# Optimization experiments

Measured on AMD Instinct MI355X. Metric: run time of the kernel, lower is better.

The kernel has to match this reference:

```python
import math
import jax, jax.numpy as jnp
import numpy as np

EPS = 1e-5
NUM_HEADER = 2


def pos_encoding(C, T, dtype):
    i = jnp.arange(C)
    exp = -((i - (i % 2)).astype(dtype) / C)
    freqs = jnp.power(jnp.asarray(10000.0, dtype), exp)[:, None]      # [C,1]
    phases = ((i % 2).astype(dtype) * (np.pi / 2))[:, None]           # [C,1]
    pos = jnp.arange(T, dtype=dtype)[None, :]                         # [1,T]
    return jnp.sin(pos * freqs + phases)                              # [C,T]


def layernorm2d(x, g, b):
    # LayerNorm over (C,T) jointly, per batch element (nn.LayerNorm([C, length]))
    mu = jnp.mean(x, axis=(1, 2), keepdims=True)
    var = jnp.mean((x - mu) ** 2, axis=(1, 2), keepdims=True)
    return (x - mu) * jax.lax.rsqrt(var + EPS) * g[None] + b[None]


def dsconv(x, dw_w, dw_b, pw_w, pw_b):
    # depthwise conv1d (groups=C, 'same' padding for odd k) + pointwise 1x1
    C = x.shape[1]
    k = dw_w.shape[-1]
    y = jax.lax.conv_general_dilated(
        x, dw_w[:, None, :], (1,), [(k // 2, k // 2)],
        dimension_numbers=('NCH', 'OIH', 'NCH'), feature_group_count=C)
    y = y + dw_b[None, :, None]
    y = jnp.einsum('bct,oc->bot', y, pw_w) + pw_b[None, :, None]
    return y


def attention(x, mask, Wq, Wk, Wv, Wo):
    # Faithful to source bug: all heads use Wqs[1]/Wks[1]/Wvs[1] -> identical heads.
    xt = jnp.transpose(x, (0, 2, 1))          # [B,T,C]
    C = xt.shape[-1]
    dk = C / NUM_HEADER
    q = xt @ Wq                               # [B,T,dk]
    k_ = xt @ Wk
    v = xt @ Wv
    s = jnp.einsum('bqd,bkd->bqk', q, k_) * (1.0 / math.sqrt(dk))
    hmask = mask[:, None, :]                  # mask over keys
    s = s * hmask + (1 - hmask) * (-1e30)
    a = jax.nn.softmax(s, axis=2) * mask[:, :, None]
    head = a @ v                              # [B,T,dk]
    heads = jnp.tile(head, (1, 1, NUM_HEADER))  # concat of identical heads
    out = heads @ Wo                          # [B,T,C]
    return jnp.transpose(out, (0, 2, 1))      # [B,C,T]


def setup_inputs() -> dict:
    key = jax.random.key(0)
    B, C, T = 16, 128, 1024
    NCONV, K = 4, 7
    dk = C // NUM_HEADER
    ks = jax.random.split(key, 12)
    inp = {
        'x': jax.random.normal(ks[0], (B, C, T), jnp.float32),
        'mask': jnp.ones((B, T), jnp.float32),
        'dw_w': jax.random.normal(ks[1], (NCONV, C, K), jnp.float32) * math.sqrt(2.0 / K),
        'dw_b': jnp.zeros((NCONV, C), jnp.float32),
        'pw_w': jax.random.normal(ks[2], (NCONV, C, C), jnp.float32) * math.sqrt(2.0 / C),
        'pw_b': jnp.zeros((NCONV, C), jnp.float32),
        'norm0_g': jnp.ones((C, T), jnp.float32),
        'norm0_b': jnp.zeros((C, T), jnp.float32),
        'norms_g': jnp.ones((NCONV, C, T), jnp.float32),
        'norms_b': jnp.zeros((NCONV, C, T), jnp.float32),
        'norme_g': jnp.ones((C, T), jnp.float32),
        'norme_b': jnp.zeros((C, T), jnp.float32),
        'Wq': jax.random.normal(ks[3], (C, dk), jnp.float32) * math.sqrt(2.0 / (C + dk)),
        'Wk': jax.random.normal(ks[4], (C, dk), jnp.float32) * math.sqrt(2.0 / (C + dk)),
        'Wv': jax.random.normal(ks[5], (C, dk), jnp.float32) * math.sqrt(2.0 / (C + dk)),
        'Wo': jax.random.normal(ks[6], (C, C), jnp.float32) * math.sqrt(2.0 / C),
        'fc_w': jax.random.normal(ks[7], (C, C), jnp.float32) * (0.1 * math.sqrt(6.0 / (2 * C))),
        'fc_b': jnp.zeros((C,), jnp.float32),
    }
    return inp


def reference(x, mask, dw_w, dw_b, pw_w, pw_b, norm0_g, norm0_b,
              norms_g, norms_b, norme_g, norme_b,
              Wq, Wk, Wv, Wo, fc_w, fc_b):
    B, C, T = x.shape
    nconv = dw_w.shape[0]
    # dropout is identity in eval mode (reference is deterministic)
    out = x + pos_encoding(C, T, x.dtype)[None]
    res = layernorm2d(out, norm0_g, norm0_b)
    for i in range(nconv):
        out = dsconv(out, dw_w[i], dw_b[i], pw_w[i], pw_b[i])
        out = jax.nn.relu(out)
        out = out + res
        res = out
        out = layernorm2d(out, norms_g[i], norms_b[i])
    out = attention(out, mask, Wq, Wk, Wv, Wo)
    out = out + res
    res = out
    out = layernorm2d(out, norme_g, norme_b)
    out = jnp.einsum('bct,oc->bot', out, fc_w) + fc_b[None, :, None]
    out = jax.nn.relu(out)
    out = out + res
    return out
```

## Files before the change

kernel.cpp:

```cpp
#include <hip/hip_runtime.h>
#include <math.h>

#define BB 16
#define CC 128
#define TT 1024
#define KK 7
#define DK 64
#define NSPLIT 4

typedef float f32x4 __attribute__((ext_vector_type(4)));
typedef short s16x8 __attribute__((ext_vector_type(8)));

__device__ inline short f2bf(float f) {
  union { float f; unsigned u; } v; v.f = f;
  unsigned r = (v.u + 0x7FFFu + ((v.u >> 16) & 1u)) >> 16;
  return (short)r;
}

__device__ inline float bf2f(short s) {
  union { unsigned u; float f; } v;
  v.u = ((unsigned)(unsigned short)s) << 16;
  return v.f;
}

__device__ inline void block_partial_256(float s, float ss, float* dst) {
#pragma unroll
  for (int off = 32; off; off >>= 1) { s += __shfl_xor(s, off); ss += __shfl_xor(ss, off); }
  __shared__ float red[8];
  int w = threadIdx.x >> 6;
  if ((threadIdx.x & 63) == 0) { red[2 * w] = s; red[2 * w + 1] = ss; }
  __syncthreads();
  if (threadIdx.x == 0) {
    for (int i = 1; i < 4; ++i) { s += red[2 * i]; ss += red[2 * i + 1]; }
    dst[0] = s; dst[1] = ss;
  }
}

__device__ inline void ln_stats_from_parts(const float* part_batch, int n, float* sh) {
  if (threadIdx.x < 64) {
    float s = 0.f, ss = 0.f;
    for (int i = threadIdx.x; i < n; i += 64) { s += part_batch[2 * i]; ss += part_batch[2 * i + 1]; }
#pragma unroll
    for (int off = 32; off; off >>= 1) { s += __shfl_xor(s, off); ss += __shfl_xor(ss, off); }
    if (threadIdx.x == 0) {
      const float invN = 1.f / (float)(CC * TT);
      float mu = s * invN;
      sh[0] = mu;
      sh[1] = rsqrtf(ss * invN - mu * mu + 1e-5f);
    }
  }
  __syncthreads();
}

__global__ __launch_bounds__(256) void k_prep(const float* __restrict__ pww,
                                              const float* __restrict__ Wq,
                                              const float* __restrict__ Wk,
                                              const float* __restrict__ Wv,
                                              const float* __restrict__ Wo,
                                              const float* __restrict__ fcw,
                                              short* __restrict__ pwwb,
                                              short* __restrict__ wqkvb,
                                              short* __restrict__ wo2b,
                                              short* __restrict__ fcwb) {
  int i = blockIdx.x * 256 + threadIdx.x;
  if (i < 65536) { pwwb[i] = f2bf(pww[i]); return; }
  i -= 65536;
  if (i < 24576) {
    int m = i >> 7, c = i & 127;
    int sel = m >> 6, d = m & 63;
    const float* srcp = sel == 0 ? Wq : (sel == 1 ? Wk : Wv);
    wqkvb[i] = f2bf(srcp[c * DK + d]);
    return;
  }
  i -= 24576;
  if (i < 8192) {
    int o = i >> 6, d = i & 63;
    wo2b[i] = f2bf(Wo[d * CC + o] + Wo[(d + 64) * CC + o]);
    return;
  }
  i -= 8192;
  fcwb[i] = f2bf(fcw[i]);
}

__global__ __launch_bounds__(256) void k_addpos(const float* __restrict__ x,
                                                float* __restrict__ out,
                                                float* __restrict__ part) {
  int bc = blockIdx.x;
  int c = bc & (CC - 1);
  float ce = (float)(c & ~1);
  float freq = expf(-(ce / (float)CC) * 9.210340371976184f);
  float phase = (c & 1) ? 1.5707963267948966f : 0.0f;
  const float* xr = x + (size_t)bc * TT;
  float* orow = out + (size_t)bc * TT;
  int t = threadIdx.x * 4;
  float4 v = *(const float4*)(xr + t);
  v.x += sinf((float)(t + 0) * freq + phase);
  v.y += sinf((float)(t + 1) * freq + phase);
  v.z += sinf((float)(t + 2) * freq + phase);
  v.w += sinf((float)(t + 3) * freq + phase);
  *(float4*)(orow + t) = v;
  float s = v.x + v.y + v.z + v.w;
  float ss = v.x * v.x + v.y * v.y + v.z * v.z + v.w * v.w;
  block_partial_256(s, ss, part + (size_t)bc * 2);
}

template <bool LN_IN, bool LN_RES>
__global__ __launch_bounds__(256) void k_dsconv(const float* __restrict__ in,
                                                const float* __restrict__ lng,
                                                const float* __restrict__ lnb,
                                                const float* __restrict__ part_in, int npart,
                                                const float* __restrict__ dww,
                                                const float* __restrict__ dwb,
                                                const short* __restrict__ pwwb,
                                                const float* __restrict__ pwb,
                                                float* __restrict__ out,
                                                float* __restrict__ part_out) {
  int tile = blockIdx.x & 31, b = blockIdx.x >> 5;
  int t0 = tile * 32;
  __shared__ float stats[2];
  __shared__ float xs[CC][41];
  __shared__ float xr2[LN_IN ? CC : 1][33];
  __shared__ __align__(16) short Dt[32][136];
  ln_stats_from_parts(part_in + (size_t)b * npart * 2, npart, stats);
  float mu = stats[0], rs = stats[1];

  for (int i = threadIdx.x; i < CC * 10; i += 256) {
    int c = i / 10, q = i - c * 10;
    int tb = t0 - 4 + q * 4;
    const float* rowp = in + ((size_t)b * CC + c) * TT;
    float r0, r1, r2, r3, o0, o1, o2, o3;
    bool full = (tb >= 0) && (tb + 4 <= TT);
    if (full) {
      float4 v = *(const float4*)(rowp + tb);
      r0 = v.x; r1 = v.y; r2 = v.z; r3 = v.w;
      o0 = r0; o1 = r1; o2 = r2; o3 = r3;
      if (LN_IN) {
        float4 g = *(const float4*)(lng + (size_t)c * TT + tb);
        float4 bv = *(const float4*)(lnb + (size_t)c * TT + tb);
        o0 = (r0 - mu) * rs * g.x + bv.x;
        o1 = (r1 - mu) * rs * g.y + bv.y;
        o2 = (r2 - mu) * rs * g.z + bv.z;
        o3 = (r3 - mu) * rs * g.w + bv.w;
      }
    } else {
      float rr[4], oo[4];
#pragma unroll
      for (int k = 0; k < 4; ++k) {
        int t = tb + k;
        bool inb = (t >= 0) && (t < TT);
        float rv = inb ? rowp[t] : 0.f;
        rr[k] = rv;
        float ov = rv;
        if (LN_IN && inb)
          ov = (rv - mu) * rs * lng[(size_t)c * TT + t] + lnb[(size_t)c * TT + t];
        oo[k] = ov;
      }
      r0 = rr[0]; r1 = rr[1]; r2 = rr[2]; r3 = rr[3];
      o0 = oo[0]; o1 = oo[1]; o2 = oo[2]; o3 = oo[3];
    }
    if (LN_IN && q >= 1 && q <= 8) {
      int tl = (q - 1) * 4;
      xr2[c][tl] = r0; xr2[c][tl + 1] = r1; xr2[c][tl + 2] = r2; xr2[c][tl + 3] = r3;
    }
    int base = q * 4;
    xs[c][base] = o0; xs[c][base + 1] = o1; xs[c][base + 2] = o2; xs[c][base + 3] = o3;
  }
  __syncthreads();
  for (int i = threadIdx.x; i < 32 * CC; i += 256) {
    int t = i >> 7, c = i & 127;
    float a = dwb[c];
#pragma unroll
    for (int j = 0; j < KK; ++j) a += dww[c * KK + j] * xs[c][t + j + 1];
    Dt[t][c] = f2bf(a);
  }
  __syncthreads();

  int w = threadIdx.x >> 6, lane = threadIdx.x & 63;
  int lo = lane & 15, hi = lane >> 4;
  f32x4 acc[2][2];
#pragma unroll
  for (int mt = 0; mt < 2; ++mt)
#pragma unroll
    for (int nt = 0; nt < 2; ++nt) { acc[mt][nt][0] = 0.f; acc[mt][nt][1] = 0.f; acc[mt][nt][2] = 0.f; acc[mt][nt][3] = 0.f; }
#pragma unroll
  for (int ks = 0; ks < 4; ++ks) {
    s16x8 b0 = *(const s16x8*)&Dt[lo][ks * 32 + hi * 8];
    s16x8 b1 = *(const s16x8*)&Dt[16 + lo][ks * 32 + hi * 8];
    s16x8 a0 = *(const s16x8*)&pwwb[(size_t)(w * 32 + lo) * CC + ks * 32 + hi * 8];
    s16x8 a1 = *(const s16x8*)&pwwb[(size_t)(w * 32 + 16 + lo) * CC + ks * 32 + hi * 8];
    acc[0][0] = __builtin_amdgcn_mfma_f32_16x16x32_bf16(a0, b0, acc[0][0], 0, 0, 0);
    acc[0][1] = __builtin_amdgcn_mfma_f32_16x16x32_bf16(a0, b1, acc[0][1], 0, 0, 0);
    acc[1][0] = __builtin_amdgcn_mfma_f32_16x16x32_bf16(a1, b0, acc[1][0], 0, 0, 0);
    acc[1][1] = __builtin_amdgcn_mfma_f32_16x16x32_bf16(a1, b1, acc[1][1], 0, 0, 0);
  }

  float s = 0.f, ss = 0.f;
#pragma unroll
  for (int mt = 0; mt < 2; ++mt)
#pragma unroll
    for (int nt = 0; nt < 2; ++nt)
#pragma unroll
      for (int r = 0; r < 4; ++r) {
        int row = w * 32 + mt * 16 + hi * 4 + r;
        int tl = nt * 16 + lo;
        int t = t0 + tl;
        float v = acc[mt][nt][r] + pwb[row];
        v = v > 0.f ? v : 0.f;
        float rv;
        if (LN_RES) {
          float raw = xs[row][tl + 4];
          rv = (raw - mu) * rs * lng[row * TT + t] + lnb[row * TT + t];
        } else if (LN_IN) {
          rv = xr2[row][tl];
        } else {
          rv = xs[row][tl + 4];
        }
        v += rv;
        out[((size_t)b * CC + row) * TT + t] = v;
        s += v; ss += v * v;
      }
  block_partial_256(s, ss, part_out + (size_t)blockIdx.x * 2);
}

__global__ __launch_bounds__(256) void k_qkv(const float* __restrict__ in,
                                             const float* __restrict__ lng,
                                             const float* __restrict__ lnb,
                                             const float* __restrict__ part_in,
                                             const short* __restrict__ wqkvb,
                                             short* __restrict__ q,
                                             short* __restrict__ k,
                                             short* __restrict__ vt) {
  int tile = blockIdx.x & 31, b = blockIdx.x >> 5;
  int t0 = tile * 32;
  __shared__ float stats[2];
  __shared__ __align__(16) short Dt[32][136];
  ln_stats_from_parts(part_in + (size_t)b * 64, 32, stats);
  float mu = stats[0], rs = stats[1];
  for (int i = threadIdx.x; i < CC * 8; i += 256) {
    int c = i >> 3, qq = i & 7;
    int t = qq * 4;
    size_t off = (size_t)c * TT + t0 + t;
    float4 v = *(const float4*)(in + (size_t)b * CC * TT + off);
    float4 g = *(const float4*)(lng + off);
    float4 bb = *(const float4*)(lnb + off);
    Dt[t + 0][c] = f2bf((v.x - mu) * rs * g.x + bb.x);
    Dt[t + 1][c] = f2bf((v.y - mu) * rs * g.y + bb.y);
    Dt[t + 2][c] = f2bf((v.z - mu) * rs * g.z + bb.z);
    Dt[t + 3][c] = f2bf((v.w - mu) * rs * g.w + bb.w);
  }
  __syncthreads();

  int w = threadIdx.x >> 6, lane = threadIdx.x & 63;
  int lo = lane & 15, hi = lane >> 4;
  f32x4 acc[3][2];
#pragma unroll
  for (int mt = 0; mt < 3; ++mt)
#pragma unroll
    for (int nt = 0; nt < 2; ++nt) { acc[mt][nt][0] = 0.f; acc[mt][nt][1] = 0.f; acc[mt][nt][2] = 0.f; acc[mt][nt][3] = 0.f; }
#pragma unroll
  for (int ks = 0; ks < 4; ++ks) {
    s16x8 b0 = *(const s16x8*)&Dt[lo][ks * 32 + hi * 8];
    s16x8 b1 = *(const s16x8*)&Dt[16 + lo][ks * 32 + hi * 8];
#pragma unroll
    for (int mt = 0; mt < 3; ++mt) {
      s16x8 a = *(const s16x8*)&wqkvb[(size_t)(w * 48 + mt * 16 + lo) * CC + ks * 32 + hi * 8];
      acc[mt][0] = __builtin_amdgcn_mfma_f32_16x16x32_bf16(a, b0, acc[mt][0], 0, 0, 0);
      acc[mt][1] = __builtin_amdgcn_mfma_f32_16x16x32_bf16(a, b1, acc[mt][1], 0, 0, 0);
    }
  }
#pragma unroll
  for (int mt = 0; mt < 3; ++mt)
#pragma unroll
    for (int nt = 0; nt < 2; ++nt) {
      int m0 = w * 48 + mt * 16 + hi * 4;
      int t = t0 + nt * 16 + lo;
      short4 pk;
      pk.x = f2bf(acc[mt][nt][0]); pk.y = f2bf(acc[mt][nt][1]);
      pk.z = f2bf(acc[mt][nt][2]); pk.w = f2bf(acc[mt][nt][3]);
      if (m0 < 64) {
        *(short4*)(q + ((size_t)b * TT + t) * DK + m0) = pk;
      } else if (m0 < 128) {
        *(short4*)(k + ((size_t)b * TT + t) * DK + (m0 - 64)) = pk;
      } else {
        int d = m0 - 128;
        vt[((size_t)b * DK + d) * TT + t] = pk.x;
        vt[((size_t)b * DK + d + 1) * TT + t] = pk.y;
        vt[((size_t)b * DK + d + 2) * TT + t] = pk.z;
        vt[((size_t)b * DK + d + 3) * TT + t] = pk.w;
      }
    }
}

__global__ __launch_bounds__(128) void k_attn(const short* __restrict__ qb,
                                              const short* __restrict__ kbuf,
                                              const short* __restrict__ vtb,
                                              const float* __restrict__ mask,
                                              short* __restrict__ pacch,
                                              float* __restrict__ pml) {
  int sp = blockIdx.x & (NSPLIT - 1);
  int qt = (blockIdx.x >> 2) & 31;
  int b = blockIdx.x >> 7;
  int w = threadIdx.x >> 6, lane = threadIdx.x & 63;
  int lo = lane & 15, hi = lane >> 4;

  __shared__ __align__(16) short ks[64][72];
  __shared__ __align__(16) short vt[64][72];
  __shared__ __align__(16) short ps[2][16][68];
  __shared__ float ms[64];

  const short* qp = qb + ((size_t)b * TT + qt * 32 + w * 16 + lo) * DK + hi * 8;
  s16x8 aq0 = *(const s16x8*)qp;
  s16x8 aq1 = *(const s16x8*)(qp + 32);

  f32x4 acc[4];
  float m_i[4], l_i[4];
#pragma unroll
  for (int r = 0; r < 4; ++r) {
    m_i[r] = -3.0e38f; l_i[r] = 0.f;
#pragma unroll
    for (int nt = 0; nt < 4; ++nt) acc[nt][r] = 0.f;
  }
  const float scale = 0.125f;

  for (int kb2 = sp * (TT / 64 / NSPLIT); kb2 < (sp + 1) * (TT / 64 / NSPLIT); ++kb2) {
    __syncthreads();
    for (int i = threadIdx.x; i < 512; i += 128) {
      int r = i >> 3, ch = i & 7;
      *(s16x8*)&ks[r][ch * 8] =
          *(const s16x8*)(kbuf + ((size_t)b * TT + kb2 * 64 + r) * DK + ch * 8);
      *(s16x8*)&vt[r][ch * 8] =
          *(const s16x8*)(vtb + ((size_t)b * DK + r) * TT + kb2 * 64 + ch * 8);
    }
    if (threadIdx.x < 64) ms[threadIdx.x] = mask[(size_t)b * TT + kb2 * 64 + threadIdx.x];
    __syncthreads();

    f32x4 sc[4];
#pragma unroll
    for (int nt = 0; nt < 4; ++nt) {
      f32x4 z; z[0] = 0.f; z[1] = 0.f; z[2] = 0.f; z[3] = 0.f;
      s16x8 bk0 = *(const s16x8*)&ks[nt * 16 + lo][hi * 8];
      s16x8 bk1 = *(const s16x8*)&ks[nt * 16 + lo][32 + hi * 8];
      z = __builtin_amdgcn_mfma_f32_16x16x32_bf16(aq0, bk0, z, 0, 0, 0);
      z = __builtin_amdgcn_mfma_f32_16x16x32_bf16(aq1, bk1, z, 0, 0, 0);
      sc[nt] = z;
    }
#pragma unroll
    for (int nt = 0; nt < 4; ++nt) {
      float mv = ms[nt * 16 + lo];
      float addv = (1.f - mv) * -1e30f;
#pragma unroll
      for (int r = 0; r < 4; ++r) sc[nt][r] = sc[nt][r] * scale * mv + addv;
    }
    float alpha[4];
#pragma unroll
    for (int r = 0; r < 4; ++r) {
      float m0 = fmaxf(fmaxf(sc[0][r], sc[1][r]), fmaxf(sc[2][r], sc[3][r]));
#pragma unroll
      for (int off = 1; off < 16; off <<= 1) m0 = fmaxf(m0, __shfl_xor(m0, off));
      float mn = fmaxf(m_i[r], m0);
      alpha[r] = __expf(m_i[r] - mn);
      m_i[r] = mn;
    }
    float psum[4] = {0.f, 0.f, 0.f, 0.f};
#pragma unroll
    for (int nt = 0; nt < 4; ++nt)
#pragma unroll
      for (int r = 0; r < 4; ++r) {
        float p = __expf(sc[nt][r] - m_i[r]);
        psum[r] += p;
        ps[w][hi * 4 + r][nt * 16 + lo] = f2bf(p);
      }
#pragma unroll
    for (int r = 0; r < 4; ++r) {
      float sum = psum[r];
#pragma unroll
      for (int off = 1; off < 16; off <<= 1) sum += __shfl_xor(sum, off);
      l_i[r] = l_i[r] * alpha[r] + sum;
    }
#pragma unroll
    for (int nt = 0; nt < 4; ++nt)
#pragma unroll
      for (int r = 0; r < 4; ++r) acc[nt][r] *= alpha[r];

    s16x8 ap0 = *(const s16x8*)&ps[w][lo][hi * 8];
    s16x8 ap1 = *(const s16x8*)&ps[w][lo][32 + hi * 8];
#pragma unroll
    for (int nt = 0; nt < 4; ++nt) {
      s16x8 bv0 = *(const s16x8*)&vt[nt * 16 + lo][hi * 8];
      s16x8 bv1 = *(const s16x8*)&vt[nt * 16 + lo][32 + hi * 8];
      acc[nt] = __builtin_amdgcn_mfma_f32_16x16x32_bf16(ap0, bv0, acc[nt], 0, 0, 0);
      acc[nt] = __builtin_amdgcn_mfma_f32_16x16x32_bf16(ap1, bv1, acc[nt], 0, 0, 0);
    }
  }
#pragma unroll
  for (int r = 0; r < 4; ++r) {
    int row = qt * 32 + w * 16 + hi * 4 + r;
    size_t pb = (((size_t)b * TT + row) * NSPLIT + sp) * DK;
#pragma unroll
    for (int nt = 0; nt < 4; ++nt) pacch[pb + nt * 16 + lo] = f2bf(acc[nt][r]);
    if (lo == 0) {
      size_t mb = (((size_t)b * TT + row) * NSPLIT + sp) * 2;
      pml[mb] = m_i[r];
      pml[mb + 1] = l_i[r];
    }
  }
}

__global__ __launch_bounds__(256) void k_attnout2(const short* __restrict__ pacch,
                                                  const float* __restrict__ pml,
                                                  const float* __restrict__ mask,
                                                  const short* __restrict__ wo2b,
                                                  const float* __restrict__ res,
                                                  float* __restrict__ out,
                                                  float* __restrict__ part_out) {
  int tile = blockIdx.x & 31, b = blockIdx.x >> 5;
  int t0 = tile * 32;
  __shared__ __align__(16) short Ht[32][72];
  {
    int i = threadIdx.x;
    int tr = i >> 3, q = i & 7;
    size_t rb = (size_t)b * TT + t0 + tr;
    float m[NSPLIT], l[NSPLIT];
#pragma unroll
    for (int s = 0; s < NSPLIT; ++s) {
      m[s] = pml[(rb * NSPLIT + s) * 2];
      l[s] = pml[(rb * NSPLIT + s) * 2 + 1];
    }
    float M = fmaxf(fmaxf(m[0], m[1]), fmaxf(m[2], m[3]));
    float wgt[NSPLIT], L = 0.f;
#pragma unroll
    for (int s = 0; s < NSPLIT; ++s) { wgt[s] = __expf(m[s] - M); L += wgt[s] * l[s]; }
    float inv = mask[rb] / L;
    float o[8] = {0.f, 0.f, 0.f, 0.f, 0.f, 0.f, 0.f, 0.f};
#pragma unroll
    for (int s = 0; s < NSPLIT; ++s) {
      s16x8 pv = *(const s16x8*)(pacch + (rb * NSPLIT + s) * DK + q * 8);
#pragma unroll
      for (int j = 0; j < 8; ++j) o[j] += wgt[s] * bf2f(pv[j]);
    }
    short h[8];
#pragma unroll
    for (int j = 0; j < 8; ++j) h[j] = f2bf(o[j] * inv);
    *(s16x8*)&Ht[tr][q * 8] = *(const s16x8*)h;
  }
  __syncthreads();

  int w = threadIdx.x >> 6, lane = threadIdx.x & 63;
  int lo = lane & 15, hi = lane >> 4;
  f32x4 acc[2][2];
#pragma unroll
  for (int mt = 0; mt < 2; ++mt)
#pragma unroll
    for (int nt = 0; nt < 2; ++nt) { acc[mt][nt][0] = 0.f; acc[mt][nt][1] = 0.f; acc[mt][nt][2] = 0.f; acc[mt][nt][3] = 0.f; }
#pragma unroll
  for (int ks = 0; ks < 2; ++ks) {
    s16x8 b0 = *(const s16x8*)&Ht[lo][ks * 32 + hi * 8];
    s16x8 b1 = *(const s16x8*)&Ht[16 + lo][ks * 32 + hi * 8];
    s16x8 a0 = *(const s16x8*)&wo2b[(size_t)(w * 32 + lo) * DK + ks * 32 + hi * 8];
    s16x8 a1 = *(const s16x8*)&wo2b[(size_t)(w * 32 + 16 + lo) * DK + ks * 32 + hi * 8];
    acc[0][0] = __builtin_amdgcn_mfma_f32_16x16x32_bf16(a0, b0, acc[0][0], 0, 0, 0);
    acc[0][1] = __builtin_amdgcn_mfma_f32_16x16x32_bf16(a0, b1, acc[0][1], 0, 0, 0);
    acc[1][0] = __builtin_amdgcn_mfma_f32_16x16x32_bf16(a1, b0, acc[1][0], 0, 0, 0);
    acc[1][1] = __builtin_amdgcn_mfma_f32_16x16x32_bf16(a1, b1, acc[1][1], 0, 0, 0);
  }
  float s = 0.f, ss = 0.f;
#pragma unroll
  for (int mt = 0; mt < 2; ++mt)
#pragma unroll
    for (int nt = 0; nt < 2; ++nt)
#pragma unroll
      for (int r = 0; r < 4; ++r) {
        int row = w * 32 + mt * 16 + hi * 4 + r;
        int t = t0 + nt * 16 + lo;
        size_t idx = ((size_t)b * CC + row) * TT + t;
        float v = acc[mt][nt][r] + res[idx];
        out[idx] = v;
        s += v; ss += v * v;
      }
  block_partial_256(s, ss, part_out + (size_t)blockIdx.x * 2);
}

__global__ __launch_bounds__(256) void k_fc(const float* __restrict__ in,
                                            const float* __restrict__ lng,
                                            const float* __restrict__ lnb,
                                            const float* __restrict__ part_in,
                                            const short* __restrict__ fcwb,
                                            const float* __restrict__ fb,
                                            float* __restrict__ out) {
  int tile = blockIdx.x & 31, b = blockIdx.x >> 5;
  int t0 = tile * 32;
  __shared__ float stats[2];
  __shared__ float xr2[CC][33];
  __shared__ __align__(16) short Dt[32][136];
  ln_stats_from_parts(part_in + (size_t)b * 64, 32, stats);
  float mu = stats[0], rs = stats[1];
  for (int i = threadIdx.x; i < CC * 8; i += 256) {
    int c = i >> 3, q = i & 7;
    int t = q * 4;
    size_t off = (size_t)c * TT + t0 + t;
    float4 v = *(const float4*)(in + (size_t)b * CC * TT + off);
    float4 g = *(const float4*)(lng + off);
    float4 bb = *(const float4*)(lnb + off);
    xr2[c][t] = v.x; xr2[c][t + 1] = v.y; xr2[c][t + 2] = v.z; xr2[c][t + 3] = v.w;
    Dt[t + 0][c] = f2bf((v.x - mu) * rs * g.x + bb.x);
    Dt[t + 1][c] = f2bf((v.y - mu) * rs * g.y + bb.y);
    Dt[t + 2][c] = f2bf((v.z - mu) * rs * g.z + bb.z);
    Dt[t + 3][c] = f2bf((v.w - mu) * rs * g.w + bb.w);
  }
  __syncthreads();

  int w = threadIdx.x >> 6, lane = threadIdx.x & 63;
  int lo = lane & 15, hi = lane >> 4;
  f32x4 acc[2][2];
#pragma unroll
  for (int mt = 0; mt < 2; ++mt)
#pragma unroll
    for (int nt = 0; nt < 2; ++nt) { acc[mt][nt][0] = 0.f; acc[mt][nt][1] = 0.f; acc[mt][nt][2] = 0.f; acc[mt][nt][3] = 0.f; }
#pragma unroll
  for (int ks = 0; ks < 4; ++ks) {
    s16x8 b0 = *(const s16x8*)&Dt[lo][ks * 32 + hi * 8];
    s16x8 b1 = *(const s16x8*)&Dt[16 + lo][ks * 32 + hi * 8];
    s16x8 a0 = *(const s16x8*)&fcwb[(size_t)(w * 32 + lo) * CC + ks * 32 + hi * 8];
    s16x8 a1 = *(const s16x8*)&fcwb[(size_t)(w * 32 + 16 + lo) * CC + ks * 32 + hi * 8];
    acc[0][0] = __builtin_amdgcn_mfma_f32_16x16x32_bf16(a0, b0, acc[0][0], 0, 0, 0);
    acc[0][1] = __builtin_amdgcn_mfma_f32_16x16x32_bf16(a0, b1, acc[0][1], 0, 0, 0);
    acc[1][0] = __builtin_amdgcn_mfma_f32_16x16x32_bf16(a1, b0, acc[1][0], 0, 0, 0);
    acc[1][1] = __builtin_amdgcn_mfma_f32_16x16x32_bf16(a1, b1, acc[1][1], 0, 0, 0);
  }
#pragma unroll
  for (int mt = 0; mt < 2; ++mt)
#pragma unroll
    for (int nt = 0; nt < 2; ++nt)
#pragma unroll
      for (int r = 0; r < 4; ++r) {
        int row = w * 32 + mt * 16 + hi * 4 + r;
        int tl = nt * 16 + lo;
        int t = t0 + tl;
        size_t idx = ((size_t)b * CC + row) * TT + t;
        float v = acc[mt][nt][r] + fb[row];
        v = v > 0.f ? v : 0.f;
        out[idx] = v + xr2[row][tl];
      }
}

extern "C" void kernel_launch(void* const* d_in, const int* in_sizes, int n_in,
                              void* d_out, int out_size, void* d_ws, size_t ws_size,
                              hipStream_t stream) {
  const float* x    = (const float*)d_in[0];
  const float* mask = (const float*)d_in[1];
  const float* dww  = (const float*)d_in[2];
  const float* dwb  = (const float*)d_in[3];
  const float* pww  = (const float*)d_in[4];
  const float* pwb  = (const float*)d_in[5];
  const float* n0g  = (const float*)d_in[6];
  const float* n0b  = (const float*)d_in[7];
  const float* nsg  = (const float*)d_in[8];
  const float* nsb  = (const float*)d_in[9];
  const float* neg_ = (const float*)d_in[10];
  const float* neb  = (const float*)d_in[11];
  const float* Wq   = (const float*)d_in[12];
  const float* Wk   = (const float*)d_in[13];
  const float* Wv   = (const float*)d_in[14];
  const float* Wo   = (const float*)d_in[15];
  const float* fcw  = (const float*)d_in[16];
  const float* fcb  = (const float*)d_in[17];
  float* out = (float*)d_out;

  float* W = (float*)d_ws;
  const size_t NBCT = (size_t)BB * CC * TT;
  const size_t NBTD = (size_t)BB * TT * DK;
  const size_t CT = (size_t)CC * TT;
  float* O     = W;
  float* S     = W + NBCT;
  float* PART0 = W + 2 * NBCT;
  float* PARTS = PART0 + 4096;
  float* PML   = PARTS + 5 * 1024;
  short* QB    = (short*)(PML + (size_t)BB * TT * NSPLIT * 2);
  short* KB    = QB + NBTD;
  short* VT    = KB + NBTD;
  short* PACCH = VT + NBTD;
  short* PWWB  = PACCH + NBTD * NSPLIT;
  short* WQKVB = PWWB + 65536;
  short* WO2B  = WQKVB + 24576;
  short* FCWB  = WO2B + 8192;

  k_prep<<<448, 256, 0, stream>>>(pww, Wq, Wk, Wv, Wo, fcw, PWWB, WQKVB, WO2B, FCWB);
  k_addpos<<<BB * CC, 256, 0, stream>>>(x, O, PART0);
  k_dsconv<false, true><<<BB * 32, 256, 0, stream>>>(
      O, n0g, n0b, PART0, 128, dww, dwb, PWWB, pwb, S, PARTS);
  k_dsconv<true, false><<<BB * 32, 256, 0, stream>>>(
      S, nsg + 0 * CT, nsb + 0 * CT, PARTS, 32,
      dww + 1 * CC * KK, dwb + 1 * CC, PWWB + 1 * CC * CC, pwb + 1 * CC, O, PARTS + 1024);
  k_dsconv<true, false><<<BB * 32, 256, 0, stream>>>(
      O, nsg + 1 * CT, nsb + 1 * CT, PARTS + 1024, 32,
      dww + 2 * CC * KK, dwb + 2 * CC, PWWB + 2 * CC * CC, pwb + 2 * CC, S, PARTS + 2048);
  k_dsconv<true, false><<<BB * 32, 256, 0, stream>>>(
      S, nsg + 2 * CT, nsb + 2 * CT, PARTS + 2048, 32,
      dww + 3 * CC * KK, dwb + 3 * CC, PWWB + 3 * CC * CC, pwb + 3 * CC, O, PARTS + 3072);
  k_qkv<<<BB * 32, 256, 0, stream>>>(O, nsg + 3 * CT, nsb + 3 * CT, PARTS + 3072,
                                     WQKVB, QB, KB, VT);
  k_attn<<<BB * 32 * NSPLIT, 128, 0, stream>>>(QB, KB, VT, mask, PACCH, PML);
  k_attnout2<<<BB * 32, 256, 0, stream>>>(PACCH, PML, mask, WO2B, O, S, PARTS + 4096);
  k_fc<<<BB * 32, 256, 0, stream>>>(S, neg_, neb, PARTS + 4096, FCWB, fcb, out);
}
```

Before: 194.2 us.

## Fuse positional add into first dsconv and coalesce epilogue stores via LDS

Merges weight prep with positional-encoding statistics into one launch, and the first dsconv recomputes x+pos on the fly, so the intermediate tensor is never written or re-read. Output stores in dsconv, qkv, attention partials, attnout and fc are staged through shared memory and written as 16-byte vectors instead of scattered scalar writes. This adds extra LDS footprint and barriers, and sin evaluations are repeated on halo elements.

```diff
diff --git a/kernel.cpp b/kernel.cpp
--- a/kernel.cpp
+++ b/kernel.cpp
@@ -52,59 +52,63 @@
   __syncthreads();
 }
 
-__global__ __launch_bounds__(256) void k_prep(const float* __restrict__ pww,
-                                              const float* __restrict__ Wq,
-                                              const float* __restrict__ Wk,
-                                              const float* __restrict__ Wv,
-                                              const float* __restrict__ Wo,
-                                              const float* __restrict__ fcw,
-                                              short* __restrict__ pwwb,
-                                              short* __restrict__ wqkvb,
-                                              short* __restrict__ wo2b,
-                                              short* __restrict__ fcwb) {
-  int i = blockIdx.x * 256 + threadIdx.x;
-  if (i < 65536) { pwwb[i] = f2bf(pww[i]); return; }
-  i -= 65536;
-  if (i < 24576) {
-    int m = i >> 7, c = i & 127;
-    int sel = m >> 6, d = m & 63;
-    const float* srcp = sel == 0 ? Wq : (sel == 1 ? Wk : Wv);
-    wqkvb[i] = f2bf(srcp[c * DK + d]);
+__global__ __launch_bounds__(256) void k_prep0(const float* __restrict__ pww,
+                                               const float* __restrict__ Wq,
+                                               const float* __restrict__ Wk,
+                                               const float* __restrict__ Wv,
+                                               const float* __restrict__ Wo,
+                                               const float* __restrict__ fcw,
+                                               const float* __restrict__ x,
+                                               short* __restrict__ pwwb,
+                                               short* __restrict__ wqkvb,
+                                               short* __restrict__ wo2b,
+                                               short* __restrict__ fcwb,
+                                               float* __restrict__ part0) {
+  if (blockIdx.x < 448) {
+    int i = blockIdx.x * 256 + threadIdx.x;
+    if (i < 65536) { pwwb[i] = f2bf(pww[i]); return; }
+    i -= 65536;
+    if (i < 24576) {
+      int m = i >> 7, c = i & 127;
+      int sel = m >> 6, d = m & 63;
+      const float* srcp = sel == 0 ? Wq : (sel == 1 ? Wk : Wv);
+      wqkvb[i] = f2bf(srcp[c * DK + d]);
+      return;
+    }
+    i -= 24576;
+    if (i < 8192) {
+      int o = i >> 6, d = i & 63;
+      wo2b[i] = f2bf(Wo[d * CC + o] + Wo[(d + 64) * CC + o]);
+      return;
+    }
+    i -= 8192;
+    fcwb[i] = f2bf(fcw[i]);
     return;
   }
-  i -= 24576;
-  if (i < 8192) {
-    int o = i >> 6, d = i & 63;
-    wo2b[i] = f2bf(Wo[d * CC + o] + Wo[(d + 64) * CC + o]);
-    return;
-  }
-  i -= 8192;
-  fcwb[i] = f2bf(fcw[i]);
-}
-
-__global__ __launch_bounds__(256) void k_addpos(const float* __restrict__ x,
-                                                float* __restrict__ out,
-                                                float* __restrict__ part) {
-  int bc = blockIdx.x;
+  int w = threadIdx.x >> 6, lane = threadIdx.x & 63;
+  int bc = (blockIdx.x - 448) * 4 + w;
   int c = bc & (CC - 1);
-  float ce = (float)(c & ~1);
-  float freq = expf(-(ce / (float)CC) * 9.210340371976184f);
-  float phase = (c & 1) ? 1.5707963267948966f : 0.0f;
+  float freq = expf(-((float)(c & ~1) * (1.f / (float)CC)) * 9.210340371976184f);
+  float ph = (c & 1) ? 1.5707963267948966f : 0.f;
   const float* xr = x + (size_t)bc * TT;
-  float* orow = out + (size_t)bc * TT;
-  int t = threadIdx.x * 4;
-  float4 v = *(const float4*)(xr + t);
-  v.x += sinf((float)(t + 0) * freq + phase);
-  v.y += sinf((float)(t + 1) * freq + phase);
-  v.z += sinf((float)(t + 2) * freq + phase);
-  v.w += sinf((float)(t + 3) * freq + phase);
-  *(float4*)(orow + t) = v;
-  float s = v.x + v.y + v.z + v.w;
-  float ss = v.x * v.x + v.y * v.y + v.z * v.z + v.w * v.w;
-  block_partial_256(s, ss, part + (size_t)bc * 2);
-}
-
-template <bool LN_IN, bool LN_RES>
+  float s = 0.f, ss = 0.f;
+#pragma unroll
+  for (int k = 0; k < 4; ++k) {
+    int t = (k * 64 + lane) * 4;
+    float4 v = *(const float4*)(xr + t);
+    v.x += sinf((float)(t + 0) * freq + ph);
+    v.y += sinf((float)(t + 1) * freq + ph);
+    v.z += sinf((float)(t + 2) * freq + ph);
+    v.w += sinf((float)(t + 3) * freq + ph);
+    s += v.x + v.y + v.z + v.w;
+    ss += v.x * v.x + v.y * v.y + v.z * v.z + v.w * v.w;
+  }
+#pragma unroll
+  for (int off = 32; off; off >>= 1) { s += __shfl_xor(s, off); ss += __shfl_xor(ss, off); }
+  if (lane == 0) { part0[(size_t)bc * 2] = s; part0[(size_t)bc * 2 + 1] = ss; }
+}
+
+template <bool LN_IN, bool LN_RES, bool ADD_POS>
 __global__ __launch_bounds__(256) void k_dsconv(const float* __restrict__ in,
                                                 const float* __restrict__ lng,
                                                 const float* __restrict__ lnb,
@@ -119,7 +123,7 @@
   int t0 = tile * 32;
   __shared__ float stats[2];
   __shared__ float xs[CC][41];
-  __shared__ float xr2[LN_IN ? CC : 1][33];
+  __shared__ float xr2[CC][33];
   __shared__ __align__(16) short Dt[32][136];
   ln_stats_from_parts(part_in + (size_t)b * npart * 2, npart, stats);
   float mu = stats[0], rs = stats[1];
@@ -128,10 +132,21 @@
     int c = i / 10, q = i - c * 10;
     int tb = t0 - 4 + q * 4;
     const float* rowp = in + ((size_t)b * CC + c) * TT;
+    float freq = 0.f, ph = 0.f;
+    if (ADD_POS) {
+      freq = expf(-((float)(c & ~1) * (1.f / (float)CC)) * 9.210340371976184f);
+      ph = (c & 1) ? 1.5707963267948966f : 0.f;
+    }
     float r0, r1, r2, r3, o0, o1, o2, o3;
     bool full = (tb >= 0) && (tb + 4 <= TT);
     if (full) {
       float4 v = *(const float4*)(rowp + tb);
+      if (ADD_POS) {
+        v.x += sinf((float)(tb + 0) * freq + ph);
+        v.y += sinf((float)(tb + 1) * freq + ph);
+        v.z += sinf((float)(tb + 2) * freq + ph);
+        v.w += sinf((float)(tb + 3) * freq + ph);
+      }
       r0 = v.x; r1 = v.y; r2 = v.z; r3 = v.w;
       o0 = r0; o1 = r1; o2 = r2; o3 = r3;
       if (LN_IN) {
@@ -148,7 +163,11 @@
       for (int k = 0; k < 4; ++k) {
         int t = tb + k;
         bool inb = (t >= 0) && (t < TT);
-        float rv = inb ? rowp[t] : 0.f;
+        float rv = 0.f;
+        if (inb) {
+          rv = rowp[t];
+          if (ADD_POS) rv += sinf((float)t * freq + ph);
+        }
         rr[k] = rv;
         float ov = rv;
         if (LN_IN && inb)
@@ -216,9 +235,17 @@
           rv = xs[row][tl + 4];
         }
         v += rv;
-        out[((size_t)b * CC + row) * TT + t] = v;
+        xr2[row][tl] = v;
         s += v; ss += v * v;
       }
+  __syncthreads();
+  for (int u = threadIdx.x; u < 1024; u += 256) {
+    int c = u >> 3, q = u & 7;
+    float4 o4;
+    o4.x = xr2[c][q * 4]; o4.y = xr2[c][q * 4 + 1];
+    o4.z = xr2[c][q * 4 + 2]; o4.w = xr2[c][q * 4 + 3];
+    *(float4*)(out + ((size_t)b * CC + c) * TT + t0 + q * 4) = o4;
+  }
   block_partial_256(s, ss, part_out + (size_t)blockIdx.x * 2);
 }
 
@@ -234,6 +261,9 @@
   int t0 = tile * 32;
   __shared__ float stats[2];
   __shared__ __align__(16) short Dt[32][136];
+  __shared__ __align__(16) short stgQ[32 * 64];
+  __shared__ __align__(16) short stgK[32 * 64];
+  __shared__ __align__(16) short stgV[64][40];
   ln_stats_from_parts(part_in + (size_t)b * 64, 32, stats);
   float mu = stats[0], rs = stats[1];
   for (int i = threadIdx.x; i < CC * 8; i += 256) {
@@ -273,22 +303,28 @@
 #pragma unroll
     for (int nt = 0; nt < 2; ++nt) {
       int m0 = w * 48 + mt * 16 + hi * 4;
-      int t = t0 + nt * 16 + lo;
-      short4 pk;
-      pk.x = f2bf(acc[mt][nt][0]); pk.y = f2bf(acc[mt][nt][1]);
-      pk.z = f2bf(acc[mt][nt][2]); pk.w = f2bf(acc[mt][nt][3]);
+      int tl = nt * 16 + lo;
+      short pv[4];
+#pragma unroll
+      for (int j = 0; j < 4; ++j) pv[j] = f2bf(acc[mt][nt][j]);
       if (m0 < 64) {
-        *(short4*)(q + ((size_t)b * TT + t) * DK + m0) = pk;
+        *(short4*)&stgQ[tl * 64 + m0] = make_short4(pv[0], pv[1], pv[2], pv[3]);
       } else if (m0 < 128) {
-        *(short4*)(k + ((size_t)b * TT + t) * DK + (m0 - 64)) = pk;
+        *(short4*)&stgK[tl * 64 + (m0 - 64)] = make_short4(pv[0], pv[1], pv[2], pv[3]);
       } else {
         int d = m0 - 128;
-        vt[((size_t)b * DK + d) * TT + t] = pk.x;
-        vt[((size_t)b * DK + d + 1) * TT + t] = pk.y;
-        vt[((size_t)b * DK + d + 2) * TT + t] = pk.z;
-        vt[((size_t)b * DK + d + 3) * TT + t] = pk.w;
-      }
-    }
+#pragma unroll
+        for (int j = 0; j < 4; ++j) stgV[d + j][tl] = pv[j];
+      }
+    }
+  __syncthreads();
+  {
+    int t = threadIdx.x >> 3, ch = threadIdx.x & 7;
+    *(s16x8*)(q + ((size_t)b * TT + t0 + t) * DK + ch * 8) = *(const s16x8*)&stgQ[t * 64 + ch * 8];
+    *(s16x8*)(k + ((size_t)b * TT + t0 + t) * DK + ch * 8) = *(const s16x8*)&stgK[t * 64 + ch * 8];
+    int d = threadIdx.x >> 2, cv = threadIdx.x & 3;
+    *(s16x8*)(vt + ((size_t)b * DK + d) * TT + t0 + cv * 8) = *(const s16x8*)&stgV[d][cv * 8];
+  }
 }
 
 __global__ __launch_bounds__(128) void k_attn(const short* __restrict__ qb,
@@ -392,17 +428,24 @@
       acc[nt] = __builtin_amdgcn_mfma_f32_16x16x32_bf16(ap1, bv1, acc[nt], 0, 0, 0);
     }
   }
+  __syncthreads();
+  short* pc = &ks[0][0];
 #pragma unroll
   for (int r = 0; r < 4; ++r) {
-    int row = qt * 32 + w * 16 + hi * 4 + r;
-    size_t pb = (((size_t)b * TT + row) * NSPLIT + sp) * DK;
-#pragma unroll
-    for (int nt = 0; nt < 4; ++nt) pacch[pb + nt * 16 + lo] = f2bf(acc[nt][r]);
+    int row = w * 16 + hi * 4 + r;
+#pragma unroll
+    for (int nt = 0; nt < 4; ++nt) pc[row * 64 + nt * 16 + lo] = f2bf(acc[nt][r]);
     if (lo == 0) {
-      size_t mb = (((size_t)b * TT + row) * NSPLIT + sp) * 2;
+      size_t mb = (((size_t)b * TT + qt * 32 + row) * NSPLIT + sp) * 2;
       pml[mb] = m_i[r];
       pml[mb + 1] = l_i[r];
     }
+  }
+  __syncthreads();
+  for (int u = threadIdx.x; u < 256; u += 128) {
+    int row = u >> 3, ch = u & 7;
+    size_t pb = (((size_t)b * TT + qt * 32 + row) * NSPLIT + sp) * DK;
+    *(s16x8*)(pacch + pb + ch * 8) = *(const s16x8*)&pc[row * 64 + ch * 8];
   }
 }
 
@@ -416,6 +459,7 @@
   int tile = blockIdx.x & 31, b = blockIdx.x >> 5;
   int t0 = tile * 32;
   __shared__ __align__(16) short Ht[32][72];
+  __shared__ float ot[128][33];
   {
     int i = threadIdx.x;
     int tr = i >> 3, q = i & 7;
@@ -471,12 +515,20 @@
 #pragma unroll
       for (int r = 0; r < 4; ++r) {
         int row = w * 32 + mt * 16 + hi * 4 + r;
-        int t = t0 + nt * 16 + lo;
-        size_t idx = ((size_t)b * CC + row) * TT + t;
+        int tl = nt * 16 + lo;
+        size_t idx = ((size_t)b * CC + row) * TT + t0 + tl;
         float v = acc[mt][nt][r] + res[idx];
-        out[idx] = v;
+        ot[row][tl] = v;
         s += v; ss += v * v;
       }
+  __syncthreads();
+  for (int u = threadIdx.x; u < 1024; u += 256) {
+    int c = u >> 3, q = u & 7;
+    float4 o4;
+    o4.x = ot[c][q * 4]; o4.y = ot[c][q * 4 + 1];
+    o4.z = ot[c][q * 4 + 2]; o4.w = ot[c][q * 4 + 3];
+    *(float4*)(out + ((size_t)b * CC + c) * TT + t0 + q * 4) = o4;
+  }
   block_partial_256(s, ss, part_out + (size_t)blockIdx.x * 2);
 }
 
@@ -535,12 +587,18 @@
       for (int r = 0; r < 4; ++r) {
         int row = w * 32 + mt * 16 + hi * 4 + r;
         int tl = nt * 16 + lo;
-        int t = t0 + tl;
-        size_t idx = ((size_t)b * CC + row) * TT + t;
         float v = acc[mt][nt][r] + fb[row];
         v = v > 0.f ? v : 0.f;
-        out[idx] = v + xr2[row][tl];
-      }
+        xr2[row][tl] = v + xr2[row][tl];
+      }
+  __syncthreads();
+  for (int u = threadIdx.x; u < 1024; u += 256) {
+    int c = u >> 3, q = u & 7;
+    float4 o4;
+    o4.x = xr2[c][q * 4]; o4.y = xr2[c][q * 4 + 1];
+    o4.z = xr2[c][q * 4 + 2]; o4.w = xr2[c][q * 4 + 3];
+    *(float4*)(out + ((size_t)b * CC + c) * TT + t0 + q * 4) = o4;
+  }
 }
 
 extern "C" void kernel_launch(void* const* d_in, const int* in_sizes, int n_in,
@@ -584,17 +642,17 @@
   short* WO2B  = WQKVB + 24576;
   short* FCWB  = WO2B + 8192;
 
-  k_prep<<<448, 256, 0, stream>>>(pww, Wq, Wk, Wv, Wo, fcw, PWWB, WQKVB, WO2B, FCWB);
-  k_addpos<<<BB * CC, 256, 0, stream>>>(x, O, PART0);
-  k_dsconv<false, true><<<BB * 32, 256, 0, stream>>>(
-      O, n0g, n0b, PART0, 128, dww, dwb, PWWB, pwb, S, PARTS);
-  k_dsconv<true, false><<<BB * 32, 256, 0, stream>>>(
+  k_prep0<<<960, 256, 0, stream>>>(pww, Wq, Wk, Wv, Wo, fcw, x,
+                                   PWWB, WQKVB, WO2B, FCWB, PART0);
+  k_dsconv<false, true, true><<<BB * 32, 256, 0, stream>>>(
+      x, n0g, n0b, PART0, 128, dww, dwb, PWWB, pwb, S, PARTS);
+  k_dsconv<true, false, false><<<BB * 32, 256, 0, stream>>>(
       S, nsg + 0 * CT, nsb + 0 * CT, PARTS, 32,
       dww + 1 * CC * KK, dwb + 1 * CC, PWWB + 1 * CC * CC, pwb + 1 * CC, O, PARTS + 1024);
-  k_dsconv<true, false><<<BB * 32, 256, 0, stream>>>(
+  k_dsconv<true, false, false><<<BB * 32, 256, 0, stream>>>(
       O, nsg + 1 * CT, nsb + 1 * CT, PARTS + 1024, 32,
       dww + 2 * CC * KK, dwb + 2 * CC, PWWB + 2 * CC * CC, pwb + 2 * CC, S, PARTS + 2048);
-  k_dsconv<true, false><<<BB * 32, 256, 0, stream>>>(
+  k_dsconv<true, false, false><<<BB * 32, 256, 0, stream>>>(
       S, nsg + 2 * CT, nsb + 2 * CT, PARTS + 2048, 32,
       dww + 3 * CC * KK, dwb + 3 * CC, PWWB + 3 * CC * CC, pwb + 3 * CC, O, PARTS + 3072);
   k_qkv<<<BB * 32, 256, 0, stream>>>(O, nsg + 3 * CT, nsb + 3 * CT, PARTS + 3072,
```

Measured after the change: 192.7 us. About the same (-0.8%).
